# Kernel optimization log

Hardware: AMD Instinct MI355X
Metric: run time of the kernel (lower is better)

## Reference

```python
import jax, jax.numpy as jnp
import numpy as np

MARGIN = 0.5


def setup_inputs() -> dict:
    key = jax.random.key(0)
    k1, k2, k3, k4 = jax.random.split(key, 4)
    Ns, Nt, D = 8192, 8192, 512
    return {
        "source_emb": jax.random.normal(k1, (Ns, D), dtype=jnp.float32),
        "target_emb": jax.random.normal(k2, (Nt, D), dtype=jnp.float32),
        "source_sec": jax.random.randint(k3, (Ns,), 0, 6),
        "target_sec": jax.random.randint(k4, (Nt,), 0, 6),
    }


def reference(source_emb, target_emb, source_sec, target_sec):
    D = source_emb.shape[-1]
    Nt = target_emb.shape[0]
    sq_s = jnp.sum(source_emb * source_emb, axis=-1)  # [Ns]
    sq_t = jnp.sum(target_emb * target_emb, axis=-1)  # [Nt]
    gram = jnp.einsum("sd,td->st", source_emb, target_emb)  # [Ns, Nt]
    d2 = jnp.maximum(sq_s[:, None] + sq_t[None, :] - 2.0 * gram, 0.0) / D
    d = jnp.sqrt(d2)
    same = source_sec[:, None] == target_sec[None, :]  # [Ns, Nt] bool
    # semantic: sum of d^2 over matching pairs, divided by Nt
    loss_s = jnp.sum(jnp.where(same, d2, 0.0), axis=1) / Nt
    # contrastive: sum of max(0, margin - d)^2 over non-matching pairs, / Nt
    hinge = jnp.maximum(0.0, MARGIN - d) ** 2
    loss_c = jnp.sum(jnp.where(same, 0.0, hinge), axis=1) / Nt
    return (loss_s, loss_c)
```

## Files before the change

kernel.cpp:

```cpp
#include <hip/hip_runtime.h>
#include <stdint.h>
#include <stddef.h>

#define NS 8192
#define NT 8192
#define DD 512
#define NSEC 6
#define QS 32.0f
#define INV_S2 (1.0f / (QS * QS))
#define INV_DNT (1.0f / ((float)DD * (float)NT))
#define INV_NT  (1.0f / (float)NT)

typedef __attribute__((ext_vector_type(4))) int i32x4;
typedef __attribute__((ext_vector_type(16))) int i32x16;

#define WS_A    ((size_t)0)
#define WS_B    (WS_A + (size_t)NS * DD)
#define WS_SQS  (WS_B + (size_t)NT * DD)
#define WS_SQT  (WS_SQS + (size_t)NS * 4)
#define WS_TS   (WS_SQT + (size_t)NT * 4)
#define WS_CNT  (WS_TS + (size_t)NSEC * DD * 4)
#define WS_SSQ  (WS_CNT + NSEC * 4)
#define WS_ZEND (WS_SSQ + NSEC * 4)

__device__ __forceinline__ void gload16(const void* g, void* l) {
  __builtin_amdgcn_global_load_lds(
      (const __attribute__((address_space(1))) unsigned int*)g,
      (__attribute__((address_space(3))) unsigned int*)l, 16, 0, 0);
}

__global__ __launch_bounds__(256) void prep_kernel(
    const float* __restrict__ src, const float* __restrict__ tgt,
    char* __restrict__ ws) {
  const int tid = threadIdx.x, wid = tid >> 6, lane = tid & 63;
  char* Ai8 = ws + WS_A;
  char* Bi8 = ws + WS_B;
  float* sqs = (float*)(ws + WS_SQS);
  float* sqt = (float*)(ws + WS_SQT);

#pragma unroll
  for (int it = 0; it < 4; ++it) {
    const int row = blockIdx.x * 4 + wid + it * 4096;
    const bool isT = row >= NS;
    const int r = isT ? row - NS : row;
    const float* in = (isT ? tgt : src) + (size_t)r * DD;
    const float4* rp = (const float4*)in;
    float4 v0 = rp[lane * 2], v1 = rp[lane * 2 + 1];
    float x[8] = {v0.x, v0.y, v0.z, v0.w, v1.x, v1.y, v1.z, v1.w};
    float ss = 0.f;
    int q[8];
#pragma unroll
    for (int j = 0; j < 8; ++j) {
      ss += x[j] * x[j];
      int qi = __float2int_rn(x[j] * QS);
      q[j] = min(127, max(-127, qi));
    }
    const int lo = (q[0] & 255) | ((q[1] & 255) << 8) |
                   ((q[2] & 255) << 16) | ((q[3] & 255) << 24);
    const int hi = (q[4] & 255) | ((q[5] & 255) << 8) |
                   ((q[6] & 255) << 16) | ((q[7] & 255) << 24);
    *(int2*)((isT ? Bi8 : Ai8) + (size_t)r * DD + lane * 8) = make_int2(lo, hi);
#pragma unroll
    for (int off = 32; off >= 1; off >>= 1) ss += __shfl_xor(ss, off, 64);
    if (lane == 0) (isT ? sqt : sqs)[r] = ss;
  }
}

__global__ __launch_bounds__(512) void tsum_kernel(
    const float* __restrict__ tgt, const int* __restrict__ tsec,
    char* __restrict__ ws) {
  const int d = threadIdx.x;
  const int r0 = blockIdx.x * 128;
  float a[NSEC] = {0.f, 0.f, 0.f, 0.f, 0.f, 0.f};
  for (int r = 0; r < 128; ++r) {
    const int sec = tsec[r0 + r];
    const float v = tgt[(size_t)(r0 + r) * DD + d];
#pragma unroll
    for (int c = 0; c < NSEC; ++c) a[c] += (sec == c) ? v : 0.f;
  }
  float* ts = (float*)(ws + WS_TS);
#pragma unroll
  for (int c = 0; c < NSEC; ++c) atomicAdd(&ts[c * DD + d], a[c]);

  if (threadIdx.x < 64) {
    const float* sqt = (const float*)(ws + WS_SQT);
    float cn[NSEC] = {0, 0, 0, 0, 0, 0}, sq[NSEC] = {0, 0, 0, 0, 0, 0};
#pragma unroll
    for (int i = 0; i < 2; ++i) {
      const int r = r0 + i * 64 + threadIdx.x;
      const int sec = tsec[r];
      const float qv = sqt[r];
#pragma unroll
      for (int c = 0; c < NSEC; ++c) {
        cn[c] += (sec == c) ? 1.f : 0.f;
        sq[c] += (sec == c) ? qv : 0.f;
      }
    }
#pragma unroll
    for (int c = 0; c < NSEC; ++c) {
#pragma unroll
      for (int off = 32; off >= 1; off >>= 1) {
        cn[c] += __shfl_xor(cn[c], off, 64);
        sq[c] += __shfl_xor(sq[c], off, 64);
      }
    }
    if (threadIdx.x == 0) {
      float* cnt = (float*)(ws + WS_CNT);
      float* ssq = (float*)(ws + WS_SSQ);
#pragma unroll
      for (int c = 0; c < NSEC; ++c) {
        atomicAdd(&cnt[c], cn[c]);
        atomicAdd(&ssq[c], sq[c]);
      }
    }
  }
}

__global__ __launch_bounds__(256) void ls_kernel(
    const float* __restrict__ src, const int* __restrict__ ssec,
    const char* __restrict__ ws, float* __restrict__ out) {
  const int tid = threadIdx.x, wid = tid >> 6, lane = tid & 63;
  const int row = blockIdx.x * 4 + wid;
  const float* tsum = (const float*)(ws + WS_TS);
  const float* cnt  = (const float*)(ws + WS_CNT);
  const float* ssq  = (const float*)(ws + WS_SSQ);
  const float* sqs  = (const float*)(ws + WS_SQS);

  const int c = ssec[row];
  const float4* rp = (const float4*)(src + (size_t)row * DD);
  const float4* tp = (const float4*)(tsum + c * DD);
  float4 a0 = rp[lane * 2], a1 = rp[lane * 2 + 1];
  float4 b0 = tp[lane * 2], b1 = tp[lane * 2 + 1];
  float dot = a0.x * b0.x + a0.y * b0.y + a0.z * b0.z + a0.w * b0.w +
              a1.x * b1.x + a1.y * b1.y + a1.z * b1.z + a1.w * b1.w;
#pragma unroll
  for (int off = 32; off >= 1; off >>= 1) dot += __shfl_xor(dot, off, 64);
  if (lane == 0)
    out[row] = (cnt[c] * sqs[row] + ssq[c] - 2.f * dot) * INV_DNT;
}

__global__ __launch_bounds__(256, 3) void gram_kernel(
    const char* __restrict__ ws, const int* __restrict__ ssec,
    const int* __restrict__ tsec, float* __restrict__ out) {
  __shared__ __align__(16) char lds[3][16384];

  const float* sqs = (const float*)(ws + WS_SQS);
  const float* sqt = (const float*)(ws + WS_SQT);

  const int lin = blockIdx.x;
  const int xcd = lin & 7, ii = lin >> 3;
  const int m_blk = xcd * 8 + (ii & 7);
  const int n_blk = ii >> 3;
  const int rowA = m_blk * 128, rowB = n_blk * 128;

  const int tid = threadIdx.x, wid = tid >> 6, lane = tid & 63;
  const int wr = wid >> 1, wc = wid & 1;
  const int lh = lane >> 5;

  const char* aSrc[2];
  const char* bSrc[2];
  int ldsDst[2];
#pragma unroll
  for (int ih = 0; ih < 2; ++ih) {
    const int o = ih * 4096 + tid * 16;
    const int row_p = o >> 6;
    const int bl = (o & 63) ^ (((row_p >> 1) & 3) << 4);
    ldsDst[ih] = ih * 4096 + wid * 1024;
    aSrc[ih] = ws + WS_A + (size_t)(rowA + row_p) * DD + bl;
    bSrc[ih] = ws + WS_B + (size_t)(rowB + row_p) * DD + bl;
  }

#define STAGE(T, BUF)                                                   \
  {                                                                     \
    gload16(aSrc[0] + (size_t)(T) * 64, &lds[BUF][ldsDst[0]]);          \
    gload16(aSrc[1] + (size_t)(T) * 64, &lds[BUF][ldsDst[1]]);          \
    gload16(bSrc[0] + (size_t)(T) * 64, &lds[BUF][8192 + ldsDst[0]]);   \
    gload16(bSrc[1] + (size_t)(T) * 64, &lds[BUF][8192 + ldsDst[1]]);   \
  }

  int aOff[2][2], bOff[2][2];
#pragma unroll
  for (int mi = 0; mi < 2; ++mi)
#pragma unroll
    for (int kk = 0; kk < 2; ++kk) {
      const int l = kk * 32 + lh * 16;
      const int ra = wr * 64 + mi * 32 + (lane & 31);
      aOff[mi][kk] = ra * 64 + (l ^ (((ra >> 1) & 3) << 4));
      const int rb = wc * 64 + mi * 32 + (lane & 31);
      bOff[mi][kk] = 8192 + rb * 64 + (l ^ (((rb >> 1) & 3) << 4));
    }

  i32x16 acc[2][2];
#pragma unroll
  for (int mi = 0; mi < 2; ++mi)
#pragma unroll
    for (int ni = 0; ni < 2; ++ni)
#pragma unroll
      for (int j = 0; j < 16; ++j) acc[mi][ni][j] = 0;

  STAGE(0, 0)
  STAGE(1, 1)
  asm volatile("s_waitcnt vmcnt(4)" ::: "memory");
  __builtin_amdgcn_sched_barrier(0);
  __builtin_amdgcn_s_barrier();

#pragma unroll
  for (int t = 0; t < 8; ++t) {
    const int cur = t % 3;
    if (t + 2 < 8) STAGE(t + 2, (t + 2) % 3)

    i32x4 a[2][2], b[2][2];
#pragma unroll
    for (int mi = 0; mi < 2; ++mi)
#pragma unroll
      for (int kk = 0; kk < 2; ++kk) {
        a[mi][kk] = *(const i32x4*)&lds[cur][aOff[mi][kk]];
        b[mi][kk] = *(const i32x4*)&lds[cur][bOff[mi][kk]];
      }
#pragma unroll
    for (int kk = 0; kk < 2; ++kk)
#pragma unroll
      for (int mi = 0; mi < 2; ++mi)
#pragma unroll
        for (int ni = 0; ni < 2; ++ni)
          acc[mi][ni] = __builtin_amdgcn_mfma_i32_32x32x32_i8(
              a[mi][kk], b[ni][kk], acc[mi][ni], 0, 0, 0);

    __builtin_amdgcn_sched_barrier(0);
    if (t + 2 < 8) {
      asm volatile("s_waitcnt vmcnt(4)" ::: "memory");
    } else if (t == 6) {
      asm volatile("s_waitcnt vmcnt(0)" ::: "memory");
    }
    __builtin_amdgcn_sched_barrier(0);
    if (t < 7) __builtin_amdgcn_s_barrier();
  }
#undef STAGE

  const int colc = lane & 31;
  float sqc[2];
#pragma unroll
  for (int ni = 0; ni < 2; ++ni)
    sqc[ni] = sqt[rowB + wc * 64 + ni * 32 + colc];

  float smin = sqs[rowA + wr * 64 + lane];
#pragma unroll
  for (int off = 32; off >= 1; off >>= 1)
    smin = fminf(smin, __shfl_xor(smin, off, 64));

  int thr[2];
#pragma unroll
  for (int ni = 0; ni < 2; ++ni)
    thr[ni] = (int)((smin + sqc[ni] - 129.0f) * 512.0f);

  int mx0 = (int)0x80000000, mx1 = (int)0x80000000;
#pragma unroll
  for (int mi = 0; mi < 2; ++mi)
#pragma unroll
    for (int j = 0; j < 16; ++j) {
      mx0 = max(mx0, acc[mi][0][j]);
      mx1 = max(mx1, acc[mi][1][j]);
    }

  if (__any((mx0 > thr[0]) || (mx1 > thr[1]))) {
#pragma unroll
    for (int mi = 0; mi < 2; ++mi) {
#pragma unroll
      for (int j = 0; j < 16; ++j) {
        const int rowin = (j & 3) + 8 * (j >> 2) + 4 * lh;
        const int grow = rowA + wr * 64 + mi * 32 + rowin;
        const float sqr = sqs[grow];
        const int sc = ssec[grow];
#pragma unroll
        for (int ni = 0; ni < 2; ++ni) {
          const int gcol = rowB + wc * 64 + ni * 32 + colc;
          const float d2r =
              sqr + sqc[ni] - 2.f * (float)acc[mi][ni][j] * INV_S2;
          if (d2r < 128.f) {
            if (sc != tsec[gcol]) {
              const float d = sqrtf(fmaxf(d2r, 0.f) * (1.f / (float)DD));
              const float hh = 0.5f - d;
              atomicAdd(&out[NS + grow], hh * hh * INV_NT);
            } else if (d2r < 0.f) {
              atomicAdd(&out[grow], -d2r * INV_DNT);
            }
          }
        }
      }
    }
  }
}

extern "C" void kernel_launch(void* const* d_in, const int* in_sizes, int n_in,
                              void* d_out, int out_size, void* d_ws, size_t ws_size,
                              hipStream_t stream) {
  const float* src = (const float*)d_in[0];
  const float* tgt = (const float*)d_in[1];
  const int* ssec = (const int*)d_in[2];
  const int* tsec = (const int*)d_in[3];
  float* out = (float*)d_out;
  char* ws = (char*)d_ws;

  hipMemsetAsync(ws + WS_TS, 0, (size_t)(WS_ZEND - WS_TS), stream);
  hipMemsetAsync(out + NS, 0, (size_t)NS * sizeof(float), stream);
  prep_kernel<<<1024, 256, 0, stream>>>(src, tgt, ws);
  tsum_kernel<<<64, 512, 0, stream>>>(tgt, tsec, ws);
  ls_kernel<<<2048, 256, 0, stream>>>(src, ssec, ws, out);
  gram_kernel<<<4096, 256, 0, stream>>>(ws, ssec, tsec, out);
}
```

Before: 86.74 us.

## Widen gram tile to 128x256 and compute semantic loss from int8 data

```diff
diff --git a/kernel.cpp b/kernel.cpp
--- a/kernel.cpp
+++ b/kernel.cpp
@@ -66,35 +66,33 @@
   }
 }
 
-__global__ __launch_bounds__(512) void tsum_kernel(
-    const float* __restrict__ tgt, const int* __restrict__ tsec,
-    char* __restrict__ ws) {
+__global__ __launch_bounds__(512) void tsumq_kernel(
+    const int* __restrict__ tsec, char* __restrict__ ws) {
   const int d = threadIdx.x;
-  const int r0 = blockIdx.x * 128;
-  float a[NSEC] = {0.f, 0.f, 0.f, 0.f, 0.f, 0.f};
-  for (int r = 0; r < 128; ++r) {
+  const int r0 = blockIdx.x * 64;
+  const signed char* B = (const signed char*)(ws + WS_B);
+  int a[NSEC] = {0, 0, 0, 0, 0, 0};
+#pragma unroll 4
+  for (int r = 0; r < 64; ++r) {
     const int sec = tsec[r0 + r];
-    const float v = tgt[(size_t)(r0 + r) * DD + d];
-#pragma unroll
-    for (int c = 0; c < NSEC; ++c) a[c] += (sec == c) ? v : 0.f;
-  }
-  float* ts = (float*)(ws + WS_TS);
-#pragma unroll
-  for (int c = 0; c < NSEC; ++c) atomicAdd(&ts[c * DD + d], a[c]);
+    const int v = (int)B[(size_t)(r0 + r) * DD + d];
+#pragma unroll
+    for (int c = 0; c < NSEC; ++c) a[c] += (sec == c) ? v : 0;
+  }
+  int* T = (int*)(ws + WS_TS);
+#pragma unroll
+  for (int c = 0; c < NSEC; ++c) atomicAdd(&T[c * DD + d], a[c]);
 
   if (threadIdx.x < 64) {
     const float* sqt = (const float*)(ws + WS_SQT);
-    float cn[NSEC] = {0, 0, 0, 0, 0, 0}, sq[NSEC] = {0, 0, 0, 0, 0, 0};
-#pragma unroll
-    for (int i = 0; i < 2; ++i) {
-      const int r = r0 + i * 64 + threadIdx.x;
-      const int sec = tsec[r];
-      const float qv = sqt[r];
-#pragma unroll
-      for (int c = 0; c < NSEC; ++c) {
-        cn[c] += (sec == c) ? 1.f : 0.f;
-        sq[c] += (sec == c) ? qv : 0.f;
-      }
+    const int r = r0 + threadIdx.x;
+    const int sec = tsec[r];
+    const float qv = sqt[r];
+    float cn[NSEC], sq[NSEC];
+#pragma unroll
+    for (int c = 0; c < NSEC; ++c) {
+      cn[c] = (sec == c) ? 1.f : 0.f;
+      sq[c] = (sec == c) ? qv : 0.f;
     }
 #pragma unroll
     for (int c = 0; c < NSEC; ++c) {
@@ -117,32 +115,38 @@
 }
 
 __global__ __launch_bounds__(256) void ls_kernel(
-    const float* __restrict__ src, const int* __restrict__ ssec,
-    const char* __restrict__ ws, float* __restrict__ out) {
+    const int* __restrict__ ssec, const char* __restrict__ ws,
+    float* __restrict__ out) {
   const int tid = threadIdx.x, wid = tid >> 6, lane = tid & 63;
   const int row = blockIdx.x * 4 + wid;
-  const float* tsum = (const float*)(ws + WS_TS);
-  const float* cnt  = (const float*)(ws + WS_CNT);
-  const float* ssq  = (const float*)(ws + WS_SSQ);
-  const float* sqs  = (const float*)(ws + WS_SQS);
-
   const int c = ssec[row];
-  const float4* rp = (const float4*)(src + (size_t)row * DD);
-  const float4* tp = (const float4*)(tsum + c * DD);
-  float4 a0 = rp[lane * 2], a1 = rp[lane * 2 + 1];
-  float4 b0 = tp[lane * 2], b1 = tp[lane * 2 + 1];
-  float dot = a0.x * b0.x + a0.y * b0.y + a0.z * b0.z + a0.w * b0.w +
-              a1.x * b1.x + a1.y * b1.y + a1.z * b1.z + a1.w * b1.w;
-#pragma unroll
-  for (int off = 32; off >= 1; off >>= 1) dot += __shfl_xor(dot, off, 64);
-  if (lane == 0)
-    out[row] = (cnt[c] * sqs[row] + ssq[c] - 2.f * dot) * INV_DNT;
-}
-
-__global__ __launch_bounds__(256, 3) void gram_kernel(
+  const signed char* A = (const signed char*)(ws + WS_A);
+  const int* T = (const int*)(ws + WS_TS) + c * DD;
+
+  union { int2 v; signed char b[8]; } u;
+  u.v = *(const int2*)(A + (size_t)row * DD + lane * 8);
+  i32x4 t0 = *(const i32x4*)(T + lane * 8);
+  i32x4 t1 = *(const i32x4*)(T + lane * 8 + 4);
+  int s = (int)u.b[0] * t0[0] + (int)u.b[1] * t0[1] +
+          (int)u.b[2] * t0[2] + (int)u.b[3] * t0[3] +
+          (int)u.b[4] * t1[0] + (int)u.b[5] * t1[1] +
+          (int)u.b[6] * t1[2] + (int)u.b[7] * t1[3];
+#pragma unroll
+  for (int off = 32; off >= 1; off >>= 1) s += __shfl_xor(s, off, 64);
+
+  if (lane == 0) {
+    const float* cnt = (const float*)(ws + WS_CNT);
+    const float* ssq = (const float*)(ws + WS_SSQ);
+    const float* sqs = (const float*)(ws + WS_SQS);
+    out[row] = (cnt[c] * sqs[row] + ssq[c] - (float)s * (1.0f / 512.0f)) *
+               INV_DNT;
+  }
+}
+
+__global__ __launch_bounds__(256, 2) void gram_kernel(
     const char* __restrict__ ws, const int* __restrict__ ssec,
     const int* __restrict__ tsec, float* __restrict__ out) {
-  __shared__ __align__(16) char lds[3][16384];
+  __shared__ __align__(16) char lds[3][24576];
 
   const float* sqs = (const float*)(ws + WS_SQS);
   const float* sqt = (const float*)(ws + WS_SQT);
@@ -151,56 +155,69 @@
   const int xcd = lin & 7, ii = lin >> 3;
   const int m_blk = xcd * 8 + (ii & 7);
   const int n_blk = ii >> 3;
-  const int rowA = m_blk * 128, rowB = n_blk * 128;
+  const int rowA = m_blk * 128, rowB = n_blk * 256;
 
   const int tid = threadIdx.x, wid = tid >> 6, lane = tid & 63;
   const int wr = wid >> 1, wc = wid & 1;
   const int lh = lane >> 5;
 
   const char* aSrc[2];
-  const char* bSrc[2];
-  int ldsDst[2];
+  const char* bSrc[4];
+  int aDst[2], bDst[4];
 #pragma unroll
   for (int ih = 0; ih < 2; ++ih) {
     const int o = ih * 4096 + tid * 16;
     const int row_p = o >> 6;
     const int bl = (o & 63) ^ (((row_p >> 1) & 3) << 4);
-    ldsDst[ih] = ih * 4096 + wid * 1024;
+    aDst[ih] = ih * 4096 + wid * 1024;
     aSrc[ih] = ws + WS_A + (size_t)(rowA + row_p) * DD + bl;
+  }
+#pragma unroll
+  for (int ih = 0; ih < 4; ++ih) {
+    const int o = ih * 4096 + tid * 16;
+    const int row_p = o >> 6;
+    const int bl = (o & 63) ^ (((row_p >> 1) & 3) << 4);
+    bDst[ih] = 8192 + ih * 4096 + wid * 1024;
     bSrc[ih] = ws + WS_B + (size_t)(rowB + row_p) * DD + bl;
   }
 
-#define STAGE(T, BUF)                                                   \
-  {                                                                     \
-    gload16(aSrc[0] + (size_t)(T) * 64, &lds[BUF][ldsDst[0]]);          \
-    gload16(aSrc[1] + (size_t)(T) * 64, &lds[BUF][ldsDst[1]]);          \
-    gload16(bSrc[0] + (size_t)(T) * 64, &lds[BUF][8192 + ldsDst[0]]);   \
-    gload16(bSrc[1] + (size_t)(T) * 64, &lds[BUF][8192 + ldsDst[1]]);   \
-  }
-
-  int aOff[2][2], bOff[2][2];
-#pragma unroll
-  for (int mi = 0; mi < 2; ++mi)
-#pragma unroll
-    for (int kk = 0; kk < 2; ++kk) {
-      const int l = kk * 32 + lh * 16;
+#define STAGE(T, BUF)                                             \
+  {                                                               \
+    gload16(aSrc[0] + (size_t)(T) * 64, &lds[BUF][aDst[0]]);      \
+    gload16(aSrc[1] + (size_t)(T) * 64, &lds[BUF][aDst[1]]);      \
+    gload16(bSrc[0] + (size_t)(T) * 64, &lds[BUF][bDst[0]]);      \
+    gload16(bSrc[1] + (size_t)(T) * 64, &lds[BUF][bDst[1]]);      \
+    gload16(bSrc[2] + (size_t)(T) * 64, &lds[BUF][bDst[2]]);      \
+    gload16(bSrc[3] + (size_t)(T) * 64, &lds[BUF][bDst[3]]);      \
+  }
+
+  int aOff[2][2], bOff[4][2];
+#pragma unroll
+  for (int kk = 0; kk < 2; ++kk) {
+    const int l = kk * 32 + lh * 16;
+#pragma unroll
+    for (int mi = 0; mi < 2; ++mi) {
       const int ra = wr * 64 + mi * 32 + (lane & 31);
       aOff[mi][kk] = ra * 64 + (l ^ (((ra >> 1) & 3) << 4));
-      const int rb = wc * 64 + mi * 32 + (lane & 31);
-      bOff[mi][kk] = 8192 + rb * 64 + (l ^ (((rb >> 1) & 3) << 4));
-    }
-
-  i32x16 acc[2][2];
+    }
+#pragma unroll
+    for (int ni = 0; ni < 4; ++ni) {
+      const int rb = wc * 128 + ni * 32 + (lane & 31);
+      bOff[ni][kk] = 8192 + rb * 64 + (l ^ (((rb >> 1) & 3) << 4));
+    }
+  }
+
+  i32x16 acc[2][4];
 #pragma unroll
   for (int mi = 0; mi < 2; ++mi)
 #pragma unroll
-    for (int ni = 0; ni < 2; ++ni)
+    for (int ni = 0; ni < 4; ++ni)
 #pragma unroll
       for (int j = 0; j < 16; ++j) acc[mi][ni][j] = 0;
 
   STAGE(0, 0)
   STAGE(1, 1)
-  asm volatile("s_waitcnt vmcnt(4)" ::: "memory");
+  asm volatile("s_waitcnt vmcnt(6)" ::: "memory");
   __builtin_amdgcn_sched_barrier(0);
   __builtin_amdgcn_s_barrier();
 
@@ -209,26 +226,28 @@
     const int cur = t % 3;
     if (t + 2 < 8) STAGE(t + 2, (t + 2) % 3)
 
-    i32x4 a[2][2], b[2][2];
-#pragma unroll
-    for (int mi = 0; mi < 2; ++mi)
-#pragma unroll
-      for (int kk = 0; kk < 2; ++kk) {
+    i32x4 a[2][2], b[4][2];
+#pragma unroll
+    for (int kk = 0; kk < 2; ++kk) {
+#pragma unroll
+      for (int mi = 0; mi < 2; ++mi)
         a[mi][kk] = *(const i32x4*)&lds[cur][aOff[mi][kk]];
-        b[mi][kk] = *(const i32x4*)&lds[cur][bOff[mi][kk]];
-      }
+#pragma unroll
+      for (int ni = 0; ni < 4; ++ni)
+        b[ni][kk] = *(const i32x4*)&lds[cur][bOff[ni][kk]];
+    }
 #pragma unroll
     for (int kk = 0; kk < 2; ++kk)
 #pragma unroll
       for (int mi = 0; mi < 2; ++mi)
 #pragma unroll
-        for (int ni = 0; ni < 2; ++ni)
+        for (int ni = 0; ni < 4; ++ni)
           acc[mi][ni] = __builtin_amdgcn_mfma_i32_32x32x32_i8(
               a[mi][kk], b[ni][kk], acc[mi][ni], 0, 0, 0);
 
     __builtin_amdgcn_sched_barrier(0);
     if (t + 2 < 8) {
-      asm volatile("s_waitcnt vmcnt(4)" ::: "memory");
+      asm volatile("s_waitcnt vmcnt(6)" ::: "memory");
     } else if (t == 6) {
       asm volatile("s_waitcnt vmcnt(0)" ::: "memory");
     }
@@ -238,31 +257,33 @@
 #undef STAGE
 
   const int colc = lane & 31;
-  float sqc[2];
-#pragma unroll
-  for (int ni = 0; ni < 2; ++ni)
-    sqc[ni] = sqt[rowB + wc * 64 + ni * 32 + colc];
+  float sqc[4];
+#pragma unroll
+  for (int ni = 0; ni < 4; ++ni)
+    sqc[ni] = sqt[rowB + wc * 128 + ni * 32 + colc];
 
   float smin = sqs[rowA + wr * 64 + lane];
 #pragma unroll
   for (int off = 32; off >= 1; off >>= 1)
     smin = fminf(smin, __shfl_xor(smin, off, 64));
 
-  int thr[2];
-#pragma unroll
-  for (int ni = 0; ni < 2; ++ni)
+  int thr[4];
+#pragma unroll
+  for (int ni = 0; ni < 4; ++ni)
     thr[ni] = (int)((smin + sqc[ni] - 129.0f) * 512.0f);
 
-  int mx0 = (int)0x80000000, mx1 = (int)0x80000000;
+  int mx[4] = {(int)0x80000000, (int)0x80000000,
+               (int)0x80000000, (int)0x80000000};
 #pragma unroll
   for (int mi = 0; mi < 2; ++mi)
 #pragma unroll
-    for (int j = 0; j < 16; ++j) {
-      mx0 = max(mx0, acc[mi][0][j]);
-      mx1 = max(mx1, acc[mi][1][j]);
-    }
-
-  if (__any((mx0 > thr[0]) || (mx1 > thr[1]))) {
+    for (int ni = 0; ni < 4; ++ni)
+#pragma unroll
+      for (int j = 0; j < 16; ++j) mx[ni] = max(mx[ni], acc[mi][ni][j]);
+
+  const bool fire = (mx[0] > thr[0]) || (mx[1] > thr[1]) ||
+                    (mx[2] > thr[2]) || (mx[3] > thr[3]);
+  if (__any(fire)) {
 #pragma unroll
     for (int mi = 0; mi < 2; ++mi) {
 #pragma unroll
@@ -272,8 +293,8 @@
         const float sqr = sqs[grow];
         const int sc = ssec[grow];
 #pragma unroll
-        for (int ni = 0; ni < 2; ++ni) {
-          const int gcol = rowB + wc * 64 + ni * 32 + colc;
+        for (int ni = 0; ni < 4; ++ni) {
+          const int gcol = rowB + wc * 128 + ni * 32 + colc;
           const float d2r =
               sqr + sqc[ni] - 2.f * (float)acc[mi][ni][j] * INV_S2;
           if (d2r < 128.f) {
@@ -304,7 +325,7 @@
   hipMemsetAsync(ws + WS_TS, 0, (size_t)(WS_ZEND - WS_TS), stream);
   hipMemsetAsync(out + NS, 0, (size_t)NS * sizeof(float), stream);
   prep_kernel<<<1024, 256, 0, stream>>>(src, tgt, ws);
-  tsum_kernel<<<64, 512, 0, stream>>>(tgt, tsec, ws);
-  ls_kernel<<<2048, 256, 0, stream>>>(src, ssec, ws, out);
-  gram_kernel<<<4096, 256, 0, stream>>>(ws, ssec, tsec, out);
-}
+  tsumq_kernel<<<128, 512, 0, stream>>>(tsec, ws);
+  ls_kernel<<<2048, 256, 0, stream>>>(ssec, ws, out);
+  gram_kernel<<<2048, 256, 0, stream>>>(ws, ssec, tsec, out);
+}
```

Result: no change. 86.44 us (-0.3%).
